# Performance work log

Hardware: AMD Instinct MI355X
Metric: run time of the kernel (lower is better)

## Reference

```python
import jax, jax.numpy as jnp
import numpy as np

EPS = 1e-05
SCALING = 1.0


def setup_inputs() -> dict:
    key = jax.random.key(0)
    k0, k1, k2, k3, k4, k5 = jax.random.split(key, 6)
    Nx = Ny = Nz = 160          # output grid resolution per axis
    D = 48                      # factor (Kronecker) rank per axis
    W = 3                       # width0: output channels (3D flow)
    NP = 2_000_000              # query points
    K = 8                       # interpolation taps per point (trilinear)
    x = jax.random.normal(k0, (Nx, D), dtype=jnp.float32)
    y = jax.random.normal(k1, (Ny, D), dtype=jnp.float32)
    z = jax.random.normal(k2, (Nz, D), dtype=jnp.float32)
    # matches torch init: 2/sqrt(W)*rand - 1/sqrt(W)
    weight = (2.0 / np.sqrt(W)) * jax.random.uniform(k3, (W, D, D, D), dtype=jnp.float32) - (1.0 / np.sqrt(W))
    B_idx = jax.random.randint(k4, (NP, K), 0, Nx * Ny * Nz, dtype=jnp.int32)
    B_w = jax.random.uniform(k5, (NP, K), dtype=jnp.float32)
    return {"x": x, "y": y, "z": z, "weight": weight, "B_idx": B_idx, "B_w": B_w}


def reference(x, y, z, weight, B_idx, B_w):
    # Tensor-mode (Kronecker) matmuls: (W,D0,D1,D2) -> (W,Nx,Ny,Nz)
    g = jnp.einsum('ap,wpqr->waqr', x, weight)   # contract mode-0
    g = jnp.einsum('bq,waqr->wabr', y, g)        # contract mode-1
    g = jnp.einsum('cr,wabr->wabc', z, g)        # contract mode-2
    # Total-variation regularizer (isotropic, per-voxel sqrt, channel-summed)
    base = g[:, :-1, :-1, :-1]
    tv = jnp.mean(
        jnp.sqrt(
            EPS
            + (g[:, :-1, :-1, 1:] - base) ** 2
            + (g[:, :-1, 1:, :-1] - base) ** 2
            + (g[:, 1:, :-1, :-1] - base) ** 2
        ).sum(axis=0)
    )
    reg_scaled = tv * SCALING
    # Gather-weighted interpolation: flat grid (Ncells, W), K taps per point
    flat = g.reshape(g.shape[0], -1).T            # (Nx*Ny*Nz, W)
    out = (flat[B_idx] * B_w[..., None]).sum(axis=1)  # (NP, W)
    return out, reg_scaled
```

## Files before the change

kernel.cpp:

```cpp
#include <hip/hip_runtime.h>
#include <hip/hip_fp16.h>

#define D 48
#define W 3
#define NX 160
#define NY 160
#define NZ 160
#define NPTS (NX*NY*NZ)
#define KNBR 8
#define EPSV 1e-5f
#define NTV (159*159*159)
#define NBTV 2048

#define T1_OFF 0
#define T1_SZ (W*NX*D*D)
#define T2_OFF (T1_OFF + T1_SZ)
#define T2_SZ (W*NX*NY*D)
#define TVP_OFF (T2_OFF + T2_SZ)
#define G3_OFF (TVP_OFF + NBTV)

__device__ inline void unpack3(uint2 u, float& f0, float& f1, float& f2) {
    __half2 lo = *reinterpret_cast<__half2*>(&u.x);
    __half2 hi = *reinterpret_cast<__half2*>(&u.y);
    f0 = __low2float(lo);
    f1 = __high2float(lo);
    f2 = __low2float(hi);
}

__global__ __launch_bounds__(256) void k1(const float* __restrict__ x,
                                          const float* __restrict__ wt,
                                          float* __restrict__ t1) {
    int lane = threadIdx.x & 63;
    int wv   = threadIdx.x >> 6;
    int q    = blockIdx.x * 4 + wv;
    int a0   = blockIdx.y * 16;
    int w    = blockIdx.z;
    bool act = lane < D;

    float wreg[D];
#pragma unroll
    for (int p = 0; p < D; ++p)
        wreg[p] = act ? wt[((w*D + p)*D + q)*D + lane] : 0.f;

    for (int ai = 0; ai < 16; ++ai) {
        int a = a0 + ai;
        const float4* xp = (const float4*)(x + a*D);
        float s = 0.f;
#pragma unroll
        for (int j = 0; j < D/4; ++j) {
            float4 xv = xp[j];
            s += xv.x * wreg[4*j+0];
            s += xv.y * wreg[4*j+1];
            s += xv.z * wreg[4*j+2];
            s += xv.w * wreg[4*j+3];
        }
        if (act) t1[((w*NX + a)*D + q)*D + lane] = s;
    }
}

__global__ __launch_bounds__(256) void k2(const float* __restrict__ y,
                                          const float* __restrict__ t1,
                                          float* __restrict__ t2) {
    int lane = threadIdx.x & 63;
    int wv   = threadIdx.x >> 6;
    int a    = blockIdx.x;
    int w    = blockIdx.y;
    bool act = lane < D;

    float t1reg[D];
    const float* t1p = t1 + ((w*NX + a)*D)*D;
#pragma unroll
    for (int q = 0; q < D; ++q)
        t1reg[q] = act ? t1p[q*D + lane] : 0.f;

    for (int bi = 0; bi < 40; ++bi) {
        int b = wv*40 + bi;
        const float4* yp = (const float4*)(y + b*D);
        float s = 0.f;
#pragma unroll
        for (int j = 0; j < D/4; ++j) {
            float4 yv = yp[j];
            s += yv.x * t1reg[4*j+0];
            s += yv.y * t1reg[4*j+1];
            s += yv.z * t1reg[4*j+2];
            s += yv.w * t1reg[4*j+3];
        }
        if (act) t2[((w*NX + a)*NY + b)*D + lane] = s;
    }
}

#define PPB 8
__global__ __launch_bounds__(192) void k3(const float* __restrict__ z,
                                          const float* __restrict__ t2,
                                          uint2* __restrict__ g3h) {
    int c = threadIdx.x;
    bool act = c < NZ;

    float zreg[D];
#pragma unroll
    for (int r = 0; r < D; ++r)
        zreg[r] = act ? z[c*D + r] : 0.f;

    int p0 = blockIdx.x * PPB;
    for (int i = 0; i < PPB; ++i) {
        int pair = p0 + i;
        int a = pair / NY, b = pair - a*NY;
        float acc[W];
#pragma unroll
        for (int w = 0; w < W; ++w) {
            const float4* t2p = (const float4*)(t2 + ((w*NX + a)*NY + b)*D);
            float s = 0.f;
#pragma unroll
            for (int j = 0; j < D/4; ++j) {
                float4 tv4 = t2p[j];
                s += tv4.x * zreg[4*j+0];
                s += tv4.y * zreg[4*j+1];
                s += tv4.z * zreg[4*j+2];
                s += tv4.w * zreg[4*j+3];
            }
            acc[w] = s;
        }
        if (act) {
            __half2 lo = __halves2half2(__float2half_rn(acc[0]), __float2half_rn(acc[1]));
            __half2 hi = __halves2half2(__float2half_rn(acc[2]), __float2half_rn(0.f));
            uint2 u;
            u.x = *reinterpret_cast<unsigned*>(&lo);
            u.y = *reinterpret_cast<unsigned*>(&hi);
            g3h[(size_t)((a*NY + b)*NZ + c)] = u;
        }
    }
}

__global__ __launch_bounds__(256) void ktv(const uint2* __restrict__ g3h,
                                           float* __restrict__ partial) {
    float v = 0.f;
    for (int t = blockIdx.x * 256 + threadIdx.x; t < NTV; t += NBTV * 256) {
        int a   = t / (159*159);
        int rem = t - a*(159*159);
        int b   = rem / 159;
        int c   = rem - b*159;
        int point = (a*NY + b)*NZ + c;
        uint2 u0 = g3h[point];
        uint2 uc = g3h[point + 1];
        uint2 ub = g3h[point + NZ];
        uint2 ua = g3h[point + NY*NZ];
        float b0,b1,b2, c0,c1,c2, d0,d1,d2, e0,e1,e2;
        unpack3(u0, b0,b1,b2);
        unpack3(uc, c0,c1,c2);
        unpack3(ub, d0,d1,d2);
        unpack3(ua, e0,e1,e2);
        float x0 = c0-b0, y0 = d0-b0, z0 = e0-b0;
        float x1 = c1-b1, y1 = d1-b1, z1 = e1-b1;
        float x2 = c2-b2, y2 = d2-b2, z2 = e2-b2;
        v += sqrtf(EPSV + x0*x0 + y0*y0 + z0*z0);
        v += sqrtf(EPSV + x1*x1 + y1*y1 + z1*z1);
        v += sqrtf(EPSV + x2*x2 + y2*y2 + z2*z2);
    }
#pragma unroll
    for (int off = 32; off > 0; off >>= 1)
        v += __shfl_down(v, off, 64);
    __shared__ float sred[4];
    int lane = threadIdx.x & 63, wv = threadIdx.x >> 6;
    if (lane == 0) sred[wv] = v;
    __syncthreads();
    if (threadIdx.x == 0)
        partial[blockIdx.x] = sred[0] + sred[1] + sred[2] + sred[3];
}

__global__ __launch_bounds__(256) void kred(const float* __restrict__ partial,
                                            float* __restrict__ outreg) {
    float v = 0.f;
    for (int i = threadIdx.x; i < NBTV; i += 256) v += partial[i];
#pragma unroll
    for (int off = 32; off > 0; off >>= 1)
        v += __shfl_down(v, off, 64);
    __shared__ float sred[4];
    int lane = threadIdx.x & 63, wv = threadIdx.x >> 6;
    if (lane == 0) sred[wv] = v;
    __syncthreads();
    if (threadIdx.x == 0)
        outreg[0] = (sred[0] + sred[1] + sred[2] + sred[3]) * (1.0f / (float)NTV);
}

__global__ __launch_bounds__(256) void kgather(const int* __restrict__ bidx,
                                               const float* __restrict__ bw,
                                               const uint2* __restrict__ g3h,
                                               float* __restrict__ out,
                                               int np) {
    int n = blockIdx.x * 256 + threadIdx.x;
    if (n >= np) return;
    const int4*   ip = (const int4*)(bidx) + (size_t)n*2;
    const float4* wp = (const float4*)(bw) + (size_t)n*2;
    int4   i0 = ip[0], i1 = ip[1];
    float4 w0 = wp[0], w1 = wp[1];
    int   ids[KNBR] = {i0.x, i0.y, i0.z, i0.w, i1.x, i1.y, i1.z, i1.w};
    float wws[KNBR] = {w0.x, w0.y, w0.z, w0.w, w1.x, w1.y, w1.z, w1.w};
    float a0 = 0.f, a1 = 0.f, a2 = 0.f;
#pragma unroll
    for (int k = 0; k < KNBR; ++k) {
        uint2 u = g3h[(size_t)ids[k]];
        float f0, f1, f2;
        unpack3(u, f0, f1, f2);
        float wk = wws[k];
        a0 += f0 * wk;
        a1 += f1 * wk;
        a2 += f2 * wk;
    }
    float* op = out + (size_t)n * 3;
    op[0] = a0; op[1] = a1; op[2] = a2;
}

extern "C" void kernel_launch(void* const* d_in, const int* in_sizes, int n_in,
                              void* d_out, int out_size, void* d_ws, size_t ws_size,
                              hipStream_t stream) {
    const float* x    = (const float*)d_in[0];
    const float* y    = (const float*)d_in[1];
    const float* z    = (const float*)d_in[2];
    const float* wt   = (const float*)d_in[3];
    const int*   bidx = (const int*)d_in[4];
    const float* bw   = (const float*)d_in[5];
    float* out = (float*)d_out;
    float* ws  = (float*)d_ws;

    float* t1  = ws + T1_OFF;
    float* t2  = ws + T2_OFF;
    float* tvp = ws + TVP_OFF;
    uint2* g3h = (uint2*)(ws + G3_OFF);
    int np = in_sizes[4] / KNBR;

    k1<<<dim3(12, 10, 3), 256, 0, stream>>>(x, wt, t1);
    k2<<<dim3(160, 3),    256, 0, stream>>>(y, t1, t2);
    k3<<<dim3(NX*NY/PPB), 192, 0, stream>>>(z, t2, g3h);

    ktv <<<dim3(NBTV), 256, 0, stream>>>(g3h, tvp);
    kred<<<dim3(1),    256, 0, stream>>>(tvp, out + (out_size - 1));

    kgather<<<dim3((np + 255) / 256), 256, 0, stream>>>(bidx, bw, g3h, out, np);
}
```

Before: 545.0 us.

## Fuse mode-1/mode-2 contractions via LDS, vectorize TV loads, two points per gather thread

Merges the y- and z-contraction kernels into one kernel that keeps the per-slab t1 and t2 intermediates in shared memory, so the large t2 buffer is never written to or read from global memory. The TV kernel now handles two adjacent c voxels per thread using 16-byte loads. The gather kernel processes two points per thread, using nontemporal loads for the streaming indices and weights and nontemporal stores for the output. The fused kernel launches only 320 blocks, so the GPU may be under-occupied, and its t2 stage recomputes work with a different access pattern.

```diff
diff --git a/kernel.cpp b/kernel.cpp
--- a/kernel.cpp
+++ b/kernel.cpp
@@ -11,12 +11,16 @@
 #define EPSV 1e-5f
 #define NTV (159*159*159)
 #define NBTV 2048
+#define TVROWS (159*159)
+#define CPAIRS 80
+#define TVSLOTS (TVROWS*CPAIRS)
+
+typedef int   vint4   __attribute__((ext_vector_type(4)));
+typedef float vfloat4 __attribute__((ext_vector_type(4)));
 
 #define T1_OFF 0
 #define T1_SZ (W*NX*D*D)
-#define T2_OFF (T1_OFF + T1_SZ)
-#define T2_SZ (W*NX*NY*D)
-#define TVP_OFF (T2_OFF + T2_SZ)
+#define TVP_OFF (T1_OFF + T1_SZ)
 #define G3_OFF (TVP_OFF + NBTV)
 
 __device__ inline void unpack3(uint2 u, float& f0, float& f1, float& f2) {
@@ -58,65 +62,64 @@
     }
 }
 
-__global__ __launch_bounds__(256) void k2(const float* __restrict__ y,
-                                          const float* __restrict__ t1,
-                                          float* __restrict__ t2) {
-    int lane = threadIdx.x & 63;
-    int wv   = threadIdx.x >> 6;
-    int a    = blockIdx.x;
-    int w    = blockIdx.y;
-    bool act = lane < D;
-
-    float t1reg[D];
-    const float* t1p = t1 + ((w*NX + a)*D)*D;
-#pragma unroll
-    for (int q = 0; q < D; ++q)
-        t1reg[q] = act ? t1p[q*D + lane] : 0.f;
-
-    for (int bi = 0; bi < 40; ++bi) {
-        int b = wv*40 + bi;
-        const float4* yp = (const float4*)(y + b*D);
-        float s = 0.f;
-#pragma unroll
-        for (int j = 0; j < D/4; ++j) {
-            float4 yv = yp[j];
-            s += yv.x * t1reg[4*j+0];
-            s += yv.y * t1reg[4*j+1];
-            s += yv.z * t1reg[4*j+2];
-            s += yv.w * t1reg[4*j+3];
-        }
-        if (act) t2[((w*NX + a)*NY + b)*D + lane] = s;
-    }
-}
-
-#define PPB 8
-__global__ __launch_bounds__(192) void k3(const float* __restrict__ z,
-                                          const float* __restrict__ t2,
-                                          uint2* __restrict__ g3h) {
-    int c = threadIdx.x;
+#define BH 80
+__global__ __launch_bounds__(192) void kbcd(const float* __restrict__ y,
+                                            const float* __restrict__ z,
+                                            const float* __restrict__ t1,
+                                            uint2* __restrict__ g3h) {
+    __shared__ float t1s[W*D*D];
+    __shared__ float t2s[W*BH*D];
+    int tid = threadIdx.x;
+    int a   = blockIdx.y;
+    int b0  = blockIdx.x * BH;
+
+    int c = tid;
     bool act = c < NZ;
-
     float zreg[D];
 #pragma unroll
-    for (int r = 0; r < D; ++r)
-        zreg[r] = act ? z[c*D + r] : 0.f;
-
-    int p0 = blockIdx.x * PPB;
-    for (int i = 0; i < PPB; ++i) {
-        int pair = p0 + i;
-        int a = pair / NY, b = pair - a*NY;
+    for (int j = 0; j < D/4; ++j) {
+        float4 zv = act ? ((const float4*)(z + c*D))[j] : make_float4(0,0,0,0);
+        zreg[4*j+0] = zv.x; zreg[4*j+1] = zv.y; zreg[4*j+2] = zv.z; zreg[4*j+3] = zv.w;
+    }
+
+    for (int i = tid; i < W*D*D; i += 192) {
+        int w = i / (D*D), rem = i - w*(D*D);
+        t1s[i] = t1[(size_t)(w*NX + a)*(D*D) + rem];
+    }
+    __syncthreads();
+
+    for (int i = tid; i < W*BH*(D/4); i += 192) {
+        int w   = i / (BH*(D/4));
+        int rem = i - w*(BH*(D/4));
+        int bh  = rem / (D/4);
+        int r4  = rem - bh*(D/4);
+        const float4* yb  = (const float4*)(y + (b0 + bh)*D);
+        const float4* t1v = (const float4*)(t1s + w*D*D) + r4;
+        float4 s = make_float4(0,0,0,0);
+#pragma unroll
+        for (int q4 = 0; q4 < D/4; ++q4) {
+            float4 yv = yb[q4];
+#pragma unroll
+            for (int u = 0; u < 4; ++u) {
+                float yq = (u==0) ? yv.x : (u==1) ? yv.y : (u==2) ? yv.z : yv.w;
+                float4 tv = t1v[(q4*4+u)*(D/4)];
+                s.x += yq*tv.x; s.y += yq*tv.y; s.z += yq*tv.z; s.w += yq*tv.w;
+            }
+        }
+        ((float4*)t2s)[i] = s;
+    }
+    __syncthreads();
+
+    for (int bh = 0; bh < BH; ++bh) {
         float acc[W];
 #pragma unroll
         for (int w = 0; w < W; ++w) {
-            const float4* t2p = (const float4*)(t2 + ((w*NX + a)*NY + b)*D);
+            const float4* t2v = (const float4*)(t2s + (w*BH + bh)*D);
             float s = 0.f;
 #pragma unroll
             for (int j = 0; j < D/4; ++j) {
-                float4 tv4 = t2p[j];
-                s += tv4.x * zreg[4*j+0];
-                s += tv4.y * zreg[4*j+1];
-                s += tv4.z * zreg[4*j+2];
-                s += tv4.w * zreg[4*j+3];
+                float4 t = t2v[j];
+                s += t.x*zreg[4*j+0] + t.y*zreg[4*j+1] + t.z*zreg[4*j+2] + t.w*zreg[4*j+3];
             }
             acc[w] = s;
         }
@@ -126,35 +129,43 @@
             uint2 u;
             u.x = *reinterpret_cast<unsigned*>(&lo);
             u.y = *reinterpret_cast<unsigned*>(&hi);
-            g3h[(size_t)((a*NY + b)*NZ + c)] = u;
-        }
-    }
+            g3h[(size_t)((a*NY + (b0+bh))*NZ + c)] = u;
+        }
+    }
+}
+
+__device__ inline float tv3(uint2 u0, uint2 uc, uint2 ub, uint2 ua) {
+    float b0,b1,b2, c0,c1,c2, d0,d1,d2, e0,e1,e2;
+    unpack3(u0,b0,b1,b2); unpack3(uc,c0,c1,c2);
+    unpack3(ub,d0,d1,d2); unpack3(ua,e0,e1,e2);
+    float x0=c0-b0, y0=d0-b0, z0=e0-b0;
+    float x1=c1-b1, y1=d1-b1, z1=e1-b1;
+    float x2=c2-b2, y2=d2-b2, z2=e2-b2;
+    return sqrtf(EPSV + x0*x0 + y0*y0 + z0*z0)
+         + sqrtf(EPSV + x1*x1 + y1*y1 + z1*z1)
+         + sqrtf(EPSV + x2*x2 + y2*y2 + z2*z2);
 }
 
 __global__ __launch_bounds__(256) void ktv(const uint2* __restrict__ g3h,
                                            float* __restrict__ partial) {
     float v = 0.f;
-    for (int t = blockIdx.x * 256 + threadIdx.x; t < NTV; t += NBTV * 256) {
-        int a   = t / (159*159);
-        int rem = t - a*(159*159);
-        int b   = rem / 159;
-        int c   = rem - b*159;
-        int point = (a*NY + b)*NZ + c;
-        uint2 u0 = g3h[point];
-        uint2 uc = g3h[point + 1];
-        uint2 ub = g3h[point + NZ];
-        uint2 ua = g3h[point + NY*NZ];
-        float b0,b1,b2, c0,c1,c2, d0,d1,d2, e0,e1,e2;
-        unpack3(u0, b0,b1,b2);
-        unpack3(uc, c0,c1,c2);
-        unpack3(ub, d0,d1,d2);
-        unpack3(ua, e0,e1,e2);
-        float x0 = c0-b0, y0 = d0-b0, z0 = e0-b0;
-        float x1 = c1-b1, y1 = d1-b1, z1 = e1-b1;
-        float x2 = c2-b2, y2 = d2-b2, z2 = e2-b2;
-        v += sqrtf(EPSV + x0*x0 + y0*y0 + z0*z0);
-        v += sqrtf(EPSV + x1*x1 + y1*y1 + z1*z1);
-        v += sqrtf(EPSV + x2*x2 + y2*y2 + z2*z2);
+    for (int s = blockIdx.x * 256 + threadIdx.x; s < TVSLOTS; s += NBTV * 256) {
+        int c2  = s % CPAIRS;
+        int row = s / CPAIRS;
+        int b   = row % 159;
+        int a   = row / 159;
+        int c   = 2*c2;
+        size_t p = (size_t)(a*NY + b)*NZ + c;
+        uint4 u0 = *(const uint4*)(g3h + p);
+        uint4 ub = *(const uint4*)(g3h + p + NZ);
+        uint4 ua = *(const uint4*)(g3h + p + NY*NZ);
+        uint2 un = g3h[p + 2];
+        uint2 u0l = make_uint2(u0.x, u0.y), u0h = make_uint2(u0.z, u0.w);
+        uint2 ubl = make_uint2(ub.x, ub.y), ubh = make_uint2(ub.z, ub.w);
+        uint2 ual = make_uint2(ua.x, ua.y), uah = make_uint2(ua.z, ua.w);
+        v += tv3(u0l, u0h, ubl, ual);
+        if (c + 1 < 159)
+            v += tv3(u0h, un, ubh, uah);
     }
 #pragma unroll
     for (int off = 32; off > 0; off >>= 1)
@@ -187,27 +198,54 @@
                                                const uint2* __restrict__ g3h,
                                                float* __restrict__ out,
                                                int np) {
-    int n = blockIdx.x * 256 + threadIdx.x;
-    if (n >= np) return;
-    const int4*   ip = (const int4*)(bidx) + (size_t)n*2;
-    const float4* wp = (const float4*)(bw) + (size_t)n*2;
-    int4   i0 = ip[0], i1 = ip[1];
-    float4 w0 = wp[0], w1 = wp[1];
-    int   ids[KNBR] = {i0.x, i0.y, i0.z, i0.w, i1.x, i1.y, i1.z, i1.w};
-    float wws[KNBR] = {w0.x, w0.y, w0.z, w0.w, w1.x, w1.y, w1.z, w1.w};
-    float a0 = 0.f, a1 = 0.f, a2 = 0.f;
+    int gid  = blockIdx.x * 256 + threadIdx.x;
+    int half = np >> 1;
+    if (gid >= half) return;
+    int n1 = gid, n2 = gid + half;
+
+    const vint4*   ip = (const vint4*)bidx;
+    const vfloat4* wp = (const vfloat4*)bw;
+    vint4   i0 = __builtin_nontemporal_load(ip + (size_t)n1*2);
+    vint4   i1 = __builtin_nontemporal_load(ip + (size_t)n1*2 + 1);
+    vint4   j0 = __builtin_nontemporal_load(ip + (size_t)n2*2);
+    vint4   j1 = __builtin_nontemporal_load(ip + (size_t)n2*2 + 1);
+    vfloat4 w0 = __builtin_nontemporal_load(wp + (size_t)n1*2);
+    vfloat4 w1 = __builtin_nontemporal_load(wp + (size_t)n1*2 + 1);
+    vfloat4 v0 = __builtin_nontemporal_load(wp + (size_t)n2*2);
+    vfloat4 v1 = __builtin_nontemporal_load(wp + (size_t)n2*2 + 1);
+
+    int   idsA[KNBR] = {i0.x, i0.y, i0.z, i0.w, i1.x, i1.y, i1.z, i1.w};
+    int   idsB[KNBR] = {j0.x, j0.y, j0.z, j0.w, j1.x, j1.y, j1.z, j1.w};
+    float wwsA[KNBR] = {w0.x, w0.y, w0.z, w0.w, w1.x, w1.y, w1.z, w1.w};
+    float wwsB[KNBR] = {v0.x, v0.y, v0.z, v0.w, v1.x, v1.y, v1.z, v1.w};
+
+    uint2 uA[KNBR], uB[KNBR];
+#pragma unroll
+    for (int k = 0; k < KNBR; ++k) uA[k] = g3h[(size_t)idsA[k]];
+#pragma unroll
+    for (int k = 0; k < KNBR; ++k) uB[k] = g3h[(size_t)idsB[k]];
+
+    float a0=0.f, a1=0.f, a2=0.f, b0=0.f, b1=0.f, b2=0.f;
 #pragma unroll
     for (int k = 0; k < KNBR; ++k) {
-        uint2 u = g3h[(size_t)ids[k]];
-        float f0, f1, f2;
-        unpack3(u, f0, f1, f2);
-        float wk = wws[k];
-        a0 += f0 * wk;
-        a1 += f1 * wk;
-        a2 += f2 * wk;
-    }
-    float* op = out + (size_t)n * 3;
-    op[0] = a0; op[1] = a1; op[2] = a2;
+        float f0,f1,f2;
+        unpack3(uA[k], f0,f1,f2);
+        a0 += f0*wwsA[k]; a1 += f1*wwsA[k]; a2 += f2*wwsA[k];
+    }
+#pragma unroll
+    for (int k = 0; k < KNBR; ++k) {
+        float f0,f1,f2;
+        unpack3(uB[k], f0,f1,f2);
+        b0 += f0*wwsB[k]; b1 += f1*wwsB[k]; b2 += f2*wwsB[k];
+    }
+    float* opA = out + (size_t)n1*3;
+    float* opB = out + (size_t)n2*3;
+    __builtin_nontemporal_store(a0, opA+0);
+    __builtin_nontemporal_store(a1, opA+1);
+    __builtin_nontemporal_store(a2, opA+2);
+    __builtin_nontemporal_store(b0, opB+0);
+    __builtin_nontemporal_store(b1, opB+1);
+    __builtin_nontemporal_store(b2, opB+2);
 }
 
 extern "C" void kernel_launch(void* const* d_in, const int* in_sizes, int n_in,
@@ -223,17 +261,15 @@
     float* ws  = (float*)d_ws;
 
     float* t1  = ws + T1_OFF;
-    float* t2  = ws + T2_OFF;
     float* tvp = ws + TVP_OFF;
     uint2* g3h = (uint2*)(ws + G3_OFF);
     int np = in_sizes[4] / KNBR;
 
-    k1<<<dim3(12, 10, 3), 256, 0, stream>>>(x, wt, t1);
-    k2<<<dim3(160, 3),    256, 0, stream>>>(y, t1, t2);
-    k3<<<dim3(NX*NY/PPB), 192, 0, stream>>>(z, t2, g3h);
+    k1  <<<dim3(12, 10, 3), 256, 0, stream>>>(x, wt, t1);
+    kbcd<<<dim3(2, NX),     192, 0, stream>>>(y, z, t1, g3h);
 
     ktv <<<dim3(NBTV), 256, 0, stream>>>(g3h, tvp);
     kred<<<dim3(1),    256, 0, stream>>>(tvp, out + (out_size - 1));
 
-    kgather<<<dim3((np + 255) / 256), 256, 0, stream>>>(bidx, bw, g3h, out, np);
-}
+    kgather<<<dim3((np/2 + 255) / 256), 256, 0, stream>>>(bidx, bw, g3h, out, np);
+}
```

Measured after the change: 524.3 us. 3.8% less time.
